# Optimization experiments

Hardware: AMD Instinct MI355X
Metric: run time of the kernel (lower is better)

The kernel has to match this reference:

```python
import jax, jax.numpy as jnp
import numpy as np

TIME_LEN = 8
JOINT_NUM = 22
SEQ = TIME_LEN * JOINT_NUM  # 176
H_NUM = 8
H_DIM = 32
NEG_BIG = -9e15


def _temporal_mask():
    # ones everywhere, except block-diagonal joint x joint blocks zeroed, plus identity
    m = np.ones((SEQ, SEQ), dtype=np.float32)
    for i in range(TIME_LEN):
        m[i * JOINT_NUM:(i + 1) * JOINT_NUM, i * JOINT_NUM:(i + 1) * JOINT_NUM] = 0.0
    spatial = 1.0 - m
    temporal = m + np.eye(SEQ, dtype=np.float32)
    return jnp.asarray(temporal), jnp.asarray(spatial)


def setup_inputs() -> dict:
    key = jax.random.key(0)
    ks = jax.random.split(key, 4)
    B, S, D_in = 256, SEQ, 128
    D_model = H_NUM * H_DIM
    s = 1.0 / np.sqrt(D_in)
    return {
        "x": jax.random.normal(ks[0], (B, S, D_in), dtype=jnp.float32),
        "Wq": jax.random.normal(ks[1], (D_in, D_model), dtype=jnp.float32) * s,
        "bq": jnp.zeros((D_model,), dtype=jnp.float32),
        "Wk": jax.random.normal(ks[2], (D_in, D_model), dtype=jnp.float32) * s,
        "bk": jnp.zeros((D_model,), dtype=jnp.float32),
        "Wv": jax.random.normal(ks[3], (D_in, D_model), dtype=jnp.float32) * s,
        "bv": jnp.zeros((D_model,), dtype=jnp.float32),
    }


def reference(x, Wq, bq, Wk, bk, Wv, bv):
    B = x.shape[0]
    mask, _ = _temporal_mask()  # att_type == 'temporal'

    def split_heads(t):  # [B,S,H*D] -> [B,H,S,D]
        return t.reshape(B, SEQ, H_NUM, H_DIM).transpose(0, 2, 1, 3)

    q = split_heads(x @ Wq + bq)
    k = split_heads(x @ Wk + bk)
    v = split_heads(jax.nn.relu(x @ Wv + bv))  # value map has ReLU

    scores = jnp.einsum("bhsd,bhtd->bhst", q, k) / jnp.sqrt(jnp.float32(H_DIM))
    scores = scores * mask + (1.0 - mask) * NEG_BIG
    att = jax.nn.softmax(scores, axis=-1)
    out = jnp.einsum("bhst,bhtd->bhsd", att, v)
    return out.transpose(0, 2, 1, 3).reshape(B, SEQ, H_NUM * H_DIM)
```

## Files before the change

kernel.cpp:

```cpp
#include <hip/hip_runtime.h>


#define SEQ    176
#define HD     32
#define DIN    128
#define DMODEL 256

typedef unsigned short ushort_t;
typedef __attribute__((ext_vector_type(8))) short short8;
typedef __attribute__((ext_vector_type(4))) short short4v;
typedef __attribute__((ext_vector_type(4))) float float4v;
typedef __attribute__((ext_vector_type(4))) unsigned short ushort4v;

#define WS_WT 0u
#define WS_X  196608u

#define SMEM_TOTAL 26496
#define OFF_KS 13056
#define OFF_VT 20096

__device__ __forceinline__ ushort_t f2bf(float f) {
    union { float f; unsigned int u; } cv; cv.f = f;
    unsigned int u = cv.u;
    unsigned int rb = 0x7FFFu + ((u >> 16) & 1u);
    return (ushort_t)((u + rb) >> 16);
}

__global__ __launch_bounds__(256)
void k0_conv(const float* __restrict__ x,
             const float* __restrict__ Wq, const float* __restrict__ Wk,
             const float* __restrict__ Wv,
             ushort_t* __restrict__ WT, ushort_t* __restrict__ X16)
{
    int bid = blockIdx.x;
    if (bid < 5632) {
        int f4 = bid * 256 + threadIdx.x;
        float4 v = reinterpret_cast<const float4*>(x)[f4];
        ushort4v o;
        o.x = f2bf(v.x); o.y = f2bf(v.y); o.z = f2bf(v.z); o.w = f2bf(v.w);
        reinterpret_cast<ushort4v*>(X16)[f4] = o;
    } else {
        int idx = (bid - 5632) * 256 + threadIdx.x;
        int e = idx * 4;
        int mat = e >> 15, h = (e >> 12) & 7, n = (e >> 7) & 31, k = e & 127;
        const float* W = (mat == 0) ? Wq : ((mat == 1) ? Wk : Wv);
        ushort4v o;
        o.x = f2bf(W[(k + 0) * DMODEL + h * HD + n]);
        o.y = f2bf(W[(k + 1) * DMODEL + h * HD + n]);
        o.z = f2bf(W[(k + 2) * DMODEL + h * HD + n]);
        o.w = f2bf(W[(k + 3) * DMODEL + h * HD + n]);
        reinterpret_cast<ushort4v*>(WT)[idx] = o;
    }
}

__global__ __launch_bounds__(704, 6)
void k1_attn(const ushort_t* __restrict__ X16, const ushort_t* __restrict__ WT,
             const float* __restrict__ bq, const float* __restrict__ bk,
             const float* __restrict__ bv, float* __restrict__ out)
{
    __shared__ ushort_t smem[SMEM_TOTAL];
    ushort_t* WS = smem;
    ushort_t* KS = smem + OFF_KS;
    ushort_t* VT = smem + OFF_VT;

    const int tid  = threadIdx.x;
    const int lane = tid & 63;
    const int w    = tid >> 6;
    const int c    = lane & 15;
    const int q    = lane >> 4;
    const int b    = blockIdx.x >> 3;
    const int h    = blockIdx.x & 7;

#pragma unroll
    for (int it = 0; it < 3; ++it) {
        int c8 = tid + it * 704;
        if (c8 < 1536) {
            int mat = c8 >> 9, rem = c8 & 511, n = rem >> 4, kc = rem & 15;
            short8 v = *reinterpret_cast<const short8*>(
                WT + (size_t)(((mat * 8 + h) * 32 + n) * 128 + kc * 8));
            *reinterpret_cast<short8*>(WS + (mat * 32 + n) * 136 + kc * 8) = v;
        }
    }
    if (tid < 512) {
        VT[(tid >> 4) * 200 + 176 + (tid & 15)] = 0;
    }
    __syncthreads();

    const ushort_t* xr = X16 + ((size_t)b * SEQ + w * 16 + c) * DIN;
    short8 xf[4];
#pragma unroll
    for (int kk = 0; kk < 4; ++kk)
        xf[kk] = *reinterpret_cast<const short8*>(xr + kk * 32 + q * 8);

    const float qscale = 0.17677669529663687f * 1.4426950408889634f;

    short8 qf8;
#pragma unroll
    for (int nt = 0; nt < 2; ++nt) {
        const ushort_t* wrow = WS + (nt * 16 + c) * 136 + q * 8;
        float4v acc = {0.f, 0.f, 0.f, 0.f};
#pragma unroll
        for (int kk = 0; kk < 4; ++kk) {
            short8 wf = *reinterpret_cast<const short8*>(wrow + kk * 32);
            acc = __builtin_amdgcn_mfma_f32_16x16x32_bf16(wf, xf[kk], acc, 0, 0, 0);
        }
        float4 bb = *reinterpret_cast<const float4*>(bq + h * HD + nt * 16 + q * 4);
        qf8[nt * 4 + 0] = (short)f2bf((acc[0] + bb.x) * qscale);
        qf8[nt * 4 + 1] = (short)f2bf((acc[1] + bb.y) * qscale);
        qf8[nt * 4 + 2] = (short)f2bf((acc[2] + bb.z) * qscale);
        qf8[nt * 4 + 3] = (short)f2bf((acc[3] + bb.w) * qscale);
    }
#pragma unroll
    for (int nt = 0; nt < 2; ++nt) {
        const ushort_t* wrow = WS + (32 + nt * 16 + c) * 136 + q * 8;
        float4v acc = {0.f, 0.f, 0.f, 0.f};
#pragma unroll
        for (int kk = 0; kk < 4; ++kk) {
            short8 wf = *reinterpret_cast<const short8*>(wrow + kk * 32);
            acc = __builtin_amdgcn_mfma_f32_16x16x32_bf16(xf[kk], wf, acc, 0, 0, 0);
        }
        float bia = bk[h * HD + nt * 16 + c];
#pragma unroll
        for (int r = 0; r < 4; ++r)
            KS[(w * 16 + q * 4 + r) * 40 + nt * 16 + c] = f2bf(acc[r] + bia);
    }
#pragma unroll
    for (int nt = 0; nt < 2; ++nt) {
        const ushort_t* wrow = WS + (64 + nt * 16 + c) * 136 + q * 8;
        float4v acc = {0.f, 0.f, 0.f, 0.f};
#pragma unroll
        for (int kk = 0; kk < 4; ++kk) {
            short8 wf = *reinterpret_cast<const short8*>(wrow + kk * 32);
            acc = __builtin_amdgcn_mfma_f32_16x16x32_bf16(wf, xf[kk], acc, 0, 0, 0);
        }
        float4 bb = *reinterpret_cast<const float4*>(bv + h * HD + nt * 16 + q * 4);
#pragma unroll
        for (int r = 0; r < 4; ++r) {
            float bias_r = (r == 0) ? bb.x : (r == 1) ? bb.y : (r == 2) ? bb.z : bb.w;
            float v = acc[r] + bias_r;
            v = v > 0.f ? v : 0.f;
            VT[(nt * 16 + q * 4 + r) * 200 + w * 16 + c] = f2bf(v);
        }
    }
    __syncthreads();

    const int t_row = w * 16 + c;
    const int lo = (t_row / 22) * 22;
    float su = 0.f;
    short8 pf[6];
    pf[5] = (short8){0, 0, 0, 0, 0, 0, 0, 0};
#pragma unroll
    for (int n = 0; n < 11; ++n) {
        const ushort_t* krow = KS + (n * 16 + c) * 40;
        short4v ka = *reinterpret_cast<const short4v*>(krow + q * 4);
        short4v kb = *reinterpret_cast<const short4v*>(krow + 16 + q * 4);
        short8 kf = {ka.x, ka.y, ka.z, ka.w, kb.x, kb.y, kb.z, kb.w};
        float4v s = {0.f, 0.f, 0.f, 0.f};
        s = __builtin_amdgcn_mfma_f32_16x16x32_bf16(kf, qf8, s, 0, 0, 0);
#pragma unroll
        for (int r = 0; r < 4; ++r) {
            int tp = n * 16 + q * 4 + r;
            float sv = (((unsigned)(tp - lo) < 22u) && (tp != t_row)) ? -1e30f : s[r];
            float e = __builtin_amdgcn_exp2f(sv);
            su += e;
            pf[n >> 1][(n & 1) * 4 + r] = (short)f2bf(e);
        }
    }
    su += __shfl_xor(su, 16, 64);
    su += __shfl_xor(su, 32, 64);
    const float invs = 1.0f / su;

    float* ob = out + ((size_t)b * SEQ + t_row) * DMODEL + h * HD;
#pragma unroll
    for (int mt = 0; mt < 2; ++mt) {
        const ushort_t* vrow = VT + (mt * 16 + c) * 200;
        float4v o = {0.f, 0.f, 0.f, 0.f};
#pragma unroll
        for (int g = 0; g < 6; ++g) {
            short4v va = *reinterpret_cast<const short4v*>(vrow + (2 * g) * 16 + q * 4);
            short4v vb = *reinterpret_cast<const short4v*>(vrow + (2 * g + 1) * 16 + q * 4);
            short8 vf = {va.x, va.y, va.z, va.w, vb.x, vb.y, vb.z, vb.w};
            o = __builtin_amdgcn_mfma_f32_16x16x32_bf16(vf, pf[g], o, 0, 0, 0);
        }
        float4 st;
        st.x = o[0] * invs; st.y = o[1] * invs;
        st.z = o[2] * invs; st.w = o[3] * invs;
        *reinterpret_cast<float4*>(ob + mt * 16 + q * 4) = st;
    }
}

extern "C" void kernel_launch(void* const* d_in, const int* in_sizes, int n_in,
                              void* d_out, int out_size, void* d_ws, size_t ws_size,
                              hipStream_t stream) {
    const float* x  = (const float*)d_in[0];
    const float* Wq = (const float*)d_in[1];
    const float* bq = (const float*)d_in[2];
    const float* Wk = (const float*)d_in[3];
    const float* bk = (const float*)d_in[4];
    const float* Wv = (const float*)d_in[5];
    const float* bv = (const float*)d_in[6];
    float* out = (float*)d_out;

    char* ws = (char*)d_ws;
    ushort_t* WT  = (ushort_t*)(ws + WS_WT);
    ushort_t* X16 = (ushort_t*)(ws + WS_X);

    k0_conv<<<dim3(5728), dim3(256), 0, stream>>>(x, Wq, Wk, Wv, WT, X16);
    k1_attn<<<dim3(2048), dim3(704), 0, stream>>>(X16, WT, bq, bk, bv, out);
}
```

Measured before the change: 133.4 us.

## Process two batches per block and swizzle K/V smem layout for 128-bit reads

Each block now handles two batch elements for one head, so the per-head weight tile is staged into shared memory once and the weight fragments are reused across both batches. K and V^T are stored with a permuted column layout so the score and PV stages can fetch each MFMA operand with a single 16-byte LDS load instead of two 8-byte loads. The grid is halved and shared memory per block grows from about 53KB to about 80KB. That may cut resident blocks per CU and adds register pressure from doubled x fragments.

```diff
diff --git a/kernel.cpp b/kernel.cpp
--- a/kernel.cpp
+++ b/kernel.cpp
@@ -15,9 +15,11 @@
 #define WS_WT 0u
 #define WS_X  196608u
 
-#define SMEM_TOTAL 26496
+#define SMEM_TOTAL 39936
 #define OFF_KS 13056
-#define OFF_VT 20096
+#define OFF_VT 27136
+#define KS_B   7040
+#define VT_B   6400
 
 __device__ __forceinline__ ushort_t f2bf(float f) {
     union { float f; unsigned int u; } cv; cv.f = f;
@@ -68,7 +70,7 @@
     const int w    = tid >> 6;
     const int c    = lane & 15;
     const int q    = lane >> 4;
-    const int b    = blockIdx.x >> 3;
+    const int b0   = (blockIdx.x >> 3) * 2;
     const int h    = blockIdx.x & 7;
 
 #pragma unroll
@@ -82,110 +84,118 @@
         }
     }
     if (tid < 512) {
-        VT[(tid >> 4) * 200 + 176 + (tid & 15)] = 0;
+        int bb = tid >> 8, rem = tid & 255;
+        int row = rem >> 3, ch = rem & 7;
+        short4v z = {0, 0, 0, 0};
+        *reinterpret_cast<short4v*>(VT + bb * VT_B + row * 200 + 160 + ch * 4) = z;
     }
     __syncthreads();
 
-    const ushort_t* xr = X16 + ((size_t)b * SEQ + w * 16 + c) * DIN;
-    short8 xf[4];
-#pragma unroll
-    for (int kk = 0; kk < 4; ++kk)
-        xf[kk] = *reinterpret_cast<const short8*>(xr + kk * 32 + q * 8);
+    short8 xf[2][4];
+#pragma unroll
+    for (int bb = 0; bb < 2; ++bb) {
+        const ushort_t* xr = X16 + ((size_t)(b0 + bb) * SEQ + w * 16 + c) * DIN;
+#pragma unroll
+        for (int kk = 0; kk < 4; ++kk)
+            xf[bb][kk] = *reinterpret_cast<const short8*>(xr + kk * 32 + q * 8);
+    }
 
     const float qscale = 0.17677669529663687f * 1.4426950408889634f;
-
-    short8 qf8;
-#pragma unroll
-    for (int nt = 0; nt < 2; ++nt) {
-        const ushort_t* wrow = WS + (nt * 16 + c) * 136 + q * 8;
-        float4v acc = {0.f, 0.f, 0.f, 0.f};
-#pragma unroll
-        for (int kk = 0; kk < 4; ++kk) {
-            short8 wf = *reinterpret_cast<const short8*>(wrow + kk * 32);
-            acc = __builtin_amdgcn_mfma_f32_16x16x32_bf16(wf, xf[kk], acc, 0, 0, 0);
-        }
-        float4 bb = *reinterpret_cast<const float4*>(bq + h * HD + nt * 16 + q * 4);
-        qf8[nt * 4 + 0] = (short)f2bf((acc[0] + bb.x) * qscale);
-        qf8[nt * 4 + 1] = (short)f2bf((acc[1] + bb.y) * qscale);
-        qf8[nt * 4 + 2] = (short)f2bf((acc[2] + bb.z) * qscale);
-        qf8[nt * 4 + 3] = (short)f2bf((acc[3] + bb.w) * qscale);
-    }
-#pragma unroll
-    for (int nt = 0; nt < 2; ++nt) {
-        const ushort_t* wrow = WS + (32 + nt * 16 + c) * 136 + q * 8;
-        float4v acc = {0.f, 0.f, 0.f, 0.f};
-#pragma unroll
-        for (int kk = 0; kk < 4; ++kk) {
-            short8 wf = *reinterpret_cast<const short8*>(wrow + kk * 32);
-            acc = __builtin_amdgcn_mfma_f32_16x16x32_bf16(xf[kk], wf, acc, 0, 0, 0);
-        }
-        float bia = bk[h * HD + nt * 16 + c];
-#pragma unroll
-        for (int r = 0; r < 4; ++r)
-            KS[(w * 16 + q * 4 + r) * 40 + nt * 16 + c] = f2bf(acc[r] + bia);
-    }
-#pragma unroll
-    for (int nt = 0; nt < 2; ++nt) {
-        const ushort_t* wrow = WS + (64 + nt * 16 + c) * 136 + q * 8;
-        float4v acc = {0.f, 0.f, 0.f, 0.f};
-#pragma unroll
-        for (int kk = 0; kk < 4; ++kk) {
-            short8 wf = *reinterpret_cast<const short8*>(wrow + kk * 32);
-            acc = __builtin_amdgcn_mfma_f32_16x16x32_bf16(wf, xf[kk], acc, 0, 0, 0);
-        }
-        float4 bb = *reinterpret_cast<const float4*>(bv + h * HD + nt * 16 + q * 4);
-#pragma unroll
-        for (int r = 0; r < 4; ++r) {
-            float bias_r = (r == 0) ? bb.x : (r == 1) ? bb.y : (r == 2) ? bb.z : bb.w;
-            float v = acc[r] + bias_r;
-            v = v > 0.f ? v : 0.f;
-            VT[(nt * 16 + q * 4 + r) * 200 + w * 16 + c] = f2bf(v);
+    short8 qf8[2];
+    const int skv = (c >> 2) * 8 + (c & 3);
+    const int svt = (w >> 1) * 32 + (c >> 2) * 8 + (w & 1) * 4 + (c & 3);
+
+#pragma unroll
+    for (int jj = 0; jj < 6; ++jj) {
+        const int mat = jj >> 1, nt = jj & 1;
+        const ushort_t* wrow = WS + (mat * 32 + nt * 16 + c) * 136 + q * 8;
+        short8 wf[4];
+#pragma unroll
+        for (int kk = 0; kk < 4; ++kk)
+            wf[kk] = *reinterpret_cast<const short8*>(wrow + kk * 32);
+
+#pragma unroll
+        for (int bb = 0; bb < 2; ++bb) {
+            float4v acc = {0.f, 0.f, 0.f, 0.f};
+            if (mat == 1) {
+#pragma unroll
+                for (int kk = 0; kk < 4; ++kk)
+                    acc = __builtin_amdgcn_mfma_f32_16x16x32_bf16(xf[bb][kk], wf[kk], acc, 0, 0, 0);
+            } else {
+#pragma unroll
+                for (int kk = 0; kk < 4; ++kk)
+                    acc = __builtin_amdgcn_mfma_f32_16x16x32_bf16(wf[kk], xf[bb][kk], acc, 0, 0, 0);
+            }
+            if (mat == 0) {
+                float4 bb4 = *reinterpret_cast<const float4*>(bq + h * HD + nt * 16 + q * 4);
+                qf8[bb][nt * 4 + 0] = (short)f2bf((acc[0] + bb4.x) * qscale);
+                qf8[bb][nt * 4 + 1] = (short)f2bf((acc[1] + bb4.y) * qscale);
+                qf8[bb][nt * 4 + 2] = (short)f2bf((acc[2] + bb4.z) * qscale);
+                qf8[bb][nt * 4 + 3] = (short)f2bf((acc[3] + bb4.w) * qscale);
+            } else if (mat == 1) {
+                float bia = bk[h * HD + nt * 16 + c];
+                ushort_t* ksb = KS + bb * KS_B;
+#pragma unroll
+                for (int r = 0; r < 4; ++r)
+                    ksb[(w * 16 + q * 4 + r) * 40 + skv + nt * 4] = f2bf(acc[r] + bia);
+            } else {
+                float4 bb4 = *reinterpret_cast<const float4*>(bv + h * HD + nt * 16 + q * 4);
+                ushort_t* vtb = VT + bb * VT_B;
+#pragma unroll
+                for (int r = 0; r < 4; ++r) {
+                    float bias_r = (r == 0) ? bb4.x : (r == 1) ? bb4.y : (r == 2) ? bb4.z : bb4.w;
+                    float v = acc[r] + bias_r;
+                    v = v > 0.f ? v : 0.f;
+                    vtb[(nt * 16 + q * 4 + r) * 200 + svt] = f2bf(v);
+                }
+            }
         }
     }
     __syncthreads();
 
     const int t_row = w * 16 + c;
     const int lo = (t_row / 22) * 22;
-    float su = 0.f;
-    short8 pf[6];
-    pf[5] = (short8){0, 0, 0, 0, 0, 0, 0, 0};
-#pragma unroll
-    for (int n = 0; n < 11; ++n) {
-        const ushort_t* krow = KS + (n * 16 + c) * 40;
-        short4v ka = *reinterpret_cast<const short4v*>(krow + q * 4);
-        short4v kb = *reinterpret_cast<const short4v*>(krow + 16 + q * 4);
-        short8 kf = {ka.x, ka.y, ka.z, ka.w, kb.x, kb.y, kb.z, kb.w};
-        float4v s = {0.f, 0.f, 0.f, 0.f};
-        s = __builtin_amdgcn_mfma_f32_16x16x32_bf16(kf, qf8, s, 0, 0, 0);
-#pragma unroll
-        for (int r = 0; r < 4; ++r) {
-            int tp = n * 16 + q * 4 + r;
-            float sv = (((unsigned)(tp - lo) < 22u) && (tp != t_row)) ? -1e30f : s[r];
-            float e = __builtin_amdgcn_exp2f(sv);
-            su += e;
-            pf[n >> 1][(n & 1) * 4 + r] = (short)f2bf(e);
-        }
-    }
-    su += __shfl_xor(su, 16, 64);
-    su += __shfl_xor(su, 32, 64);
-    const float invs = 1.0f / su;
-
-    float* ob = out + ((size_t)b * SEQ + t_row) * DMODEL + h * HD;
-#pragma unroll
-    for (int mt = 0; mt < 2; ++mt) {
-        const ushort_t* vrow = VT + (mt * 16 + c) * 200;
-        float4v o = {0.f, 0.f, 0.f, 0.f};
-#pragma unroll
-        for (int g = 0; g < 6; ++g) {
-            short4v va = *reinterpret_cast<const short4v*>(vrow + (2 * g) * 16 + q * 4);
-            short4v vb = *reinterpret_cast<const short4v*>(vrow + (2 * g + 1) * 16 + q * 4);
-            short8 vf = {va.x, va.y, va.z, va.w, vb.x, vb.y, vb.z, vb.w};
-            o = __builtin_amdgcn_mfma_f32_16x16x32_bf16(vf, pf[g], o, 0, 0, 0);
-        }
-        float4 st;
-        st.x = o[0] * invs; st.y = o[1] * invs;
-        st.z = o[2] * invs; st.w = o[3] * invs;
-        *reinterpret_cast<float4*>(ob + mt * 16 + q * 4) = st;
+
+#pragma unroll
+    for (int bb = 0; bb < 2; ++bb) {
+        const ushort_t* KSb = KS + bb * KS_B;
+        const ushort_t* VTb = VT + bb * VT_B;
+        float su = 0.f;
+        short8 pf[6];
+        pf[5] = (short8){0, 0, 0, 0, 0, 0, 0, 0};
+#pragma unroll
+        for (int n = 0; n < 11; ++n) {
+            short8 kf = *reinterpret_cast<const short8*>(KSb + (n * 16 + c) * 40 + q * 8);
+            float4v s = {0.f, 0.f, 0.f, 0.f};
+            s = __builtin_amdgcn_mfma_f32_16x16x32_bf16(kf, qf8[bb], s, 0, 0, 0);
+#pragma unroll
+            for (int r = 0; r < 4; ++r) {
+                int tp = n * 16 + q * 4 + r;
+                float sv = (((unsigned)(tp - lo) < 22u) && (tp != t_row)) ? -1e30f : s[r];
+                float e = __builtin_amdgcn_exp2f(sv);
+                su += e;
+                pf[n >> 1][(n & 1) * 4 + r] = (short)f2bf(e);
+            }
+        }
+        su += __shfl_xor(su, 16, 64);
+        su += __shfl_xor(su, 32, 64);
+        const float invs = 1.0f / su;
+
+        float* ob = out + ((size_t)(b0 + bb) * SEQ + t_row) * DMODEL + h * HD;
+#pragma unroll
+        for (int mt = 0; mt < 2; ++mt) {
+            const ushort_t* vrow = VTb + (mt * 16 + c) * 200;
+            float4v o = {0.f, 0.f, 0.f, 0.f};
+#pragma unroll
+            for (int g = 0; g < 6; ++g) {
+                short8 vf = *reinterpret_cast<const short8*>(vrow + g * 32 + q * 8);
+                o = __builtin_amdgcn_mfma_f32_16x16x32_bf16(vf, pf[g], o, 0, 0, 0);
+            }
+            float4 st;
+            st.x = o[0] * invs; st.y = o[1] * invs;
+            st.z = o[2] * invs; st.w = o[3] * invs;
+            *reinterpret_cast<float4*>(ob + mt * 16 + q * 4) = st;
+        }
     }
 }
 
@@ -206,5 +216,5 @@
     ushort_t* X16 = (ushort_t*)(ws + WS_X);
 
     k0_conv<<<dim3(5728), dim3(256), 0, stream>>>(x, Wq, Wk, Wv, WT, X16);
-    k1_attn<<<dim3(2048), dim3(704), 0, stream>>>(X16, WT, bq, bk, bv, out);
-}
+    k1_attn<<<dim3(1024), dim3(704), 0, stream>>>(X16, WT, bq, bk, bv, out);
+}
```

New measurement: 135.9 us. No clear change (+1.8%).

## Shrink attention blocks to 8 waves, read weights from global, permute K/V LDS layout

Applied to the files above, without the earlier changes.

The attention kernel now runs 512-thread blocks. Each wave handles up to two 16-row tiles, with the 11 tiles spread over 8 waves. The per-block LDS copy of the weight slices is dropped, and weights are read directly from global/L2, roughly halving shared memory per block. K and V are stored in a permuted LDS layout so that score and PV fragments load as single 16-byte reads instead of two 8-byte reads. Blocks are reordered so consecutive blocks share a head, and a cheaper round-half-up bf16 conversion is used inside the attention kernel. The trade-off is less balanced work (some waves do two tiles, others one) and more global weight traffic in exchange for higher occupancy and fewer LDS operations.

```diff
diff --git a/kernel.cpp b/kernel.cpp
--- a/kernel.cpp
+++ b/kernel.cpp
@@ -15,15 +15,18 @@
 #define WS_WT 0u
 #define WS_X  196608u
 
-#define SMEM_TOTAL 26496
-#define OFF_KS 13056
-#define OFF_VT 20096
-
-__device__ __forceinline__ ushort_t f2bf(float f) {
+#define SMEM_TOTAL 13440
+#define OFF_VT 7040
+
+__device__ __forceinline__ ushort_t f2bf_rtne(float f) {
     union { float f; unsigned int u; } cv; cv.f = f;
     unsigned int u = cv.u;
     unsigned int rb = 0x7FFFu + ((u >> 16) & 1u);
     return (ushort_t)((u + rb) >> 16);
+}
+__device__ __forceinline__ ushort_t f2bf(float f) {
+    union { float f; unsigned int u; } cv; cv.f = f;
+    return (ushort_t)((cv.u + 0x8000u) >> 16);
 }
 
 __global__ __launch_bounds__(256)
@@ -37,7 +40,8 @@
         int f4 = bid * 256 + threadIdx.x;
         float4 v = reinterpret_cast<const float4*>(x)[f4];
         ushort4v o;
-        o.x = f2bf(v.x); o.y = f2bf(v.y); o.z = f2bf(v.z); o.w = f2bf(v.w);
+        o.x = f2bf_rtne(v.x); o.y = f2bf_rtne(v.y);
+        o.z = f2bf_rtne(v.z); o.w = f2bf_rtne(v.w);
         reinterpret_cast<ushort4v*>(X16)[f4] = o;
     } else {
         int idx = (bid - 5632) * 256 + threadIdx.x;
@@ -45,147 +49,140 @@
         int mat = e >> 15, h = (e >> 12) & 7, n = (e >> 7) & 31, k = e & 127;
         const float* W = (mat == 0) ? Wq : ((mat == 1) ? Wk : Wv);
         ushort4v o;
-        o.x = f2bf(W[(k + 0) * DMODEL + h * HD + n]);
-        o.y = f2bf(W[(k + 1) * DMODEL + h * HD + n]);
-        o.z = f2bf(W[(k + 2) * DMODEL + h * HD + n]);
-        o.w = f2bf(W[(k + 3) * DMODEL + h * HD + n]);
+        o.x = f2bf_rtne(W[(k + 0) * DMODEL + h * HD + n]);
+        o.y = f2bf_rtne(W[(k + 1) * DMODEL + h * HD + n]);
+        o.z = f2bf_rtne(W[(k + 2) * DMODEL + h * HD + n]);
+        o.w = f2bf_rtne(W[(k + 3) * DMODEL + h * HD + n]);
         reinterpret_cast<ushort4v*>(WT)[idx] = o;
     }
 }
 
-__global__ __launch_bounds__(704, 6)
+__global__ __launch_bounds__(512, 8)
 void k1_attn(const ushort_t* __restrict__ X16, const ushort_t* __restrict__ WT,
              const float* __restrict__ bq, const float* __restrict__ bk,
              const float* __restrict__ bv, float* __restrict__ out)
 {
     __shared__ ushort_t smem[SMEM_TOTAL];
-    ushort_t* WS = smem;
-    ushort_t* KS = smem + OFF_KS;
+    ushort_t* KS = smem;
     ushort_t* VT = smem + OFF_VT;
 
     const int tid  = threadIdx.x;
     const int lane = tid & 63;
-    const int w    = tid >> 6;
+    const int wave = tid >> 6;
     const int c    = lane & 15;
     const int q    = lane >> 4;
-    const int b    = blockIdx.x >> 3;
-    const int h    = blockIdx.x & 7;
-
-#pragma unroll
-    for (int it = 0; it < 3; ++it) {
-        int c8 = tid + it * 704;
-        if (c8 < 1536) {
-            int mat = c8 >> 9, rem = c8 & 511, n = rem >> 4, kc = rem & 15;
-            short8 v = *reinterpret_cast<const short8*>(
-                WT + (size_t)(((mat * 8 + h) * 32 + n) * 128 + kc * 8));
-            *reinterpret_cast<short8*>(WS + (mat * 32 + n) * 136 + kc * 8) = v;
+    const int b    = blockIdx.x & 255;
+    const int h    = blockIdx.x >> 8;
+
+    {
+        int row = tid >> 4, m = tid & 15;
+        VT[row * 200 + 160 + (m >> 2) * 8 + 4 + (m & 3)] = 0;
+    }
+
+    const float qscale = 0.17677669529663687f * 1.4426950408889634f;
+    const int skv = (c >> 2) * 8 + (c & 3);
+    short8 qf8[2];
+
+#pragma unroll
+    for (int it = 0; it < 2; ++it) {
+        const int mt = wave + it * 8;
+        if (mt < 11) {
+            const ushort_t* xr = X16 + ((size_t)b * SEQ + mt * 16 + c) * DIN;
+            short8 xf[4];
+#pragma unroll
+            for (int kk = 0; kk < 4; ++kk)
+                xf[kk] = *reinterpret_cast<const short8*>(xr + kk * 32 + q * 8);
+            const int svt = (mt >> 1) * 32 + (c >> 2) * 8 + (mt & 1) * 4 + (c & 3);
+
+#pragma unroll
+            for (int jj = 0; jj < 6; ++jj) {
+                const int mat = jj >> 1, nt = jj & 1;
+                const ushort_t* wrow =
+                    WT + (size_t)(((mat * 8 + h) * 32 + nt * 16 + c)) * 128 + q * 8;
+                float4v acc = {0.f, 0.f, 0.f, 0.f};
+                if (mat == 1) {
+#pragma unroll
+                    for (int kk = 0; kk < 4; ++kk) {
+                        short8 wf = *reinterpret_cast<const short8*>(wrow + kk * 32);
+                        acc = __builtin_amdgcn_mfma_f32_16x16x32_bf16(xf[kk], wf, acc, 0, 0, 0);
+                    }
+                } else {
+#pragma unroll
+                    for (int kk = 0; kk < 4; ++kk) {
+                        short8 wf = *reinterpret_cast<const short8*>(wrow + kk * 32);
+                        acc = __builtin_amdgcn_mfma_f32_16x16x32_bf16(wf, xf[kk], acc, 0, 0, 0);
+                    }
+                }
+                if (mat == 0) {
+                    float4 bb4 = *reinterpret_cast<const float4*>(bq + h * HD + nt * 16 + q * 4);
+                    qf8[it][nt * 4 + 0] = (short)f2bf((acc[0] + bb4.x) * qscale);
+                    qf8[it][nt * 4 + 1] = (short)f2bf((acc[1] + bb4.y) * qscale);
+                    qf8[it][nt * 4 + 2] = (short)f2bf((acc[2] + bb4.z) * qscale);
+                    qf8[it][nt * 4 + 3] = (short)f2bf((acc[3] + bb4.w) * qscale);
+                } else if (mat == 1) {
+                    float bia = bk[h * HD + nt * 16 + c];
+#pragma unroll
+                    for (int r = 0; r < 4; ++r)
+                        KS[(mt * 16 + q * 4 + r) * 40 + skv + nt * 4] = f2bf(acc[r] + bia);
+                } else {
+                    float4 bb4 = *reinterpret_cast<const float4*>(bv + h * HD + nt * 16 + q * 4);
+#pragma unroll
+                    for (int r = 0; r < 4; ++r) {
+                        float bias_r = (r == 0) ? bb4.x : (r == 1) ? bb4.y
+                                      : (r == 2) ? bb4.z : bb4.w;
+                        float v = acc[r] + bias_r;
+                        v = v > 0.f ? v : 0.f;
+                        VT[(nt * 16 + q * 4 + r) * 200 + svt] = f2bf(v);
+                    }
+                }
+            }
         }
     }
-    if (tid < 512) {
-        VT[(tid >> 4) * 200 + 176 + (tid & 15)] = 0;
-    }
     __syncthreads();
 
-    const ushort_t* xr = X16 + ((size_t)b * SEQ + w * 16 + c) * DIN;
-    short8 xf[4];
-#pragma unroll
-    for (int kk = 0; kk < 4; ++kk)
-        xf[kk] = *reinterpret_cast<const short8*>(xr + kk * 32 + q * 8);
-
-    const float qscale = 0.17677669529663687f * 1.4426950408889634f;
-
-    short8 qf8;
-#pragma unroll
-    for (int nt = 0; nt < 2; ++nt) {
-        const ushort_t* wrow = WS + (nt * 16 + c) * 136 + q * 8;
-        float4v acc = {0.f, 0.f, 0.f, 0.f};
-#pragma unroll
-        for (int kk = 0; kk < 4; ++kk) {
-            short8 wf = *reinterpret_cast<const short8*>(wrow + kk * 32);
-            acc = __builtin_amdgcn_mfma_f32_16x16x32_bf16(wf, xf[kk], acc, 0, 0, 0);
+#pragma unroll
+    for (int it = 0; it < 2; ++it) {
+        const int rt = wave + it * 8;
+        if (rt < 11) {
+            const int t_row = rt * 16 + c;
+            const int lo = (t_row / 22) * 22;
+            float su = 0.f;
+            short8 pf[6];
+            pf[5] = (short8){0, 0, 0, 0, 0, 0, 0, 0};
+#pragma unroll
+            for (int n = 0; n < 11; ++n) {
+                short8 kf = *reinterpret_cast<const short8*>(KS + (n * 16 + c) * 40 + q * 8);
+                float4v s = {0.f, 0.f, 0.f, 0.f};
+                s = __builtin_amdgcn_mfma_f32_16x16x32_bf16(kf, qf8[it], s, 0, 0, 0);
+#pragma unroll
+                for (int r = 0; r < 4; ++r) {
+                    int tp = n * 16 + q * 4 + r;
+                    float sv = (((unsigned)(tp - lo) < 22u) && (tp != t_row)) ? -1e30f : s[r];
+                    float e = __builtin_amdgcn_exp2f(sv);
+                    su += e;
+                    pf[n >> 1][(n & 1) * 4 + r] = (short)f2bf(e);
+                }
+            }
+            su += __shfl_xor(su, 16, 64);
+            su += __shfl_xor(su, 32, 64);
+            const float invs = 1.0f / su;
+
+            float* ob = out + ((size_t)b * SEQ + t_row) * DMODEL + h * HD;
+#pragma unroll
+            for (int mt2 = 0; mt2 < 2; ++mt2) {
+                const ushort_t* vrow = VT + (mt2 * 16 + c) * 200;
+                float4v o = {0.f, 0.f, 0.f, 0.f};
+#pragma unroll
+                for (int g = 0; g < 6; ++g) {
+                    short8 vf = *reinterpret_cast<const short8*>(vrow + g * 32 + q * 8);
+                    o = __builtin_amdgcn_mfma_f32_16x16x32_bf16(vf, pf[g], o, 0, 0, 0);
+                }
+                float4 st;
+                st.x = o[0] * invs; st.y = o[1] * invs;
+                st.z = o[2] * invs; st.w = o[3] * invs;
+                *reinterpret_cast<float4*>(ob + mt2 * 16 + q * 4) = st;
+            }
         }
-        float4 bb = *reinterpret_cast<const float4*>(bq + h * HD + nt * 16 + q * 4);
-        qf8[nt * 4 + 0] = (short)f2bf((acc[0] + bb.x) * qscale);
-        qf8[nt * 4 + 1] = (short)f2bf((acc[1] + bb.y) * qscale);
-        qf8[nt * 4 + 2] = (short)f2bf((acc[2] + bb.z) * qscale);
-        qf8[nt * 4 + 3] = (short)f2bf((acc[3] + bb.w) * qscale);
-    }
-#pragma unroll
-    for (int nt = 0; nt < 2; ++nt) {
-        const ushort_t* wrow = WS + (32 + nt * 16 + c) * 136 + q * 8;
-        float4v acc = {0.f, 0.f, 0.f, 0.f};
-#pragma unroll
-        for (int kk = 0; kk < 4; ++kk) {
-            short8 wf = *reinterpret_cast<const short8*>(wrow + kk * 32);
-            acc = __builtin_amdgcn_mfma_f32_16x16x32_bf16(xf[kk], wf, acc, 0, 0, 0);
-        }
-        float bia = bk[h * HD + nt * 16 + c];
-#pragma unroll
-        for (int r = 0; r < 4; ++r)
-            KS[(w * 16 + q * 4 + r) * 40 + nt * 16 + c] = f2bf(acc[r] + bia);
-    }
-#pragma unroll
-    for (int nt = 0; nt < 2; ++nt) {
-        const ushort_t* wrow = WS + (64 + nt * 16 + c) * 136 + q * 8;
-        float4v acc = {0.f, 0.f, 0.f, 0.f};
-#pragma unroll
-        for (int kk = 0; kk < 4; ++kk) {
-            short8 wf = *reinterpret_cast<const short8*>(wrow + kk * 32);
-            acc = __builtin_amdgcn_mfma_f32_16x16x32_bf16(wf, xf[kk], acc, 0, 0, 0);
-        }
-        float4 bb = *reinterpret_cast<const float4*>(bv + h * HD + nt * 16 + q * 4);
-#pragma unroll
-        for (int r = 0; r < 4; ++r) {
-            float bias_r = (r == 0) ? bb.x : (r == 1) ? bb.y : (r == 2) ? bb.z : bb.w;
-            float v = acc[r] + bias_r;
-            v = v > 0.f ? v : 0.f;
-            VT[(nt * 16 + q * 4 + r) * 200 + w * 16 + c] = f2bf(v);
-        }
-    }
-    __syncthreads();
-
-    const int t_row = w * 16 + c;
-    const int lo = (t_row / 22) * 22;
-    float su = 0.f;
-    short8 pf[6];
-    pf[5] = (short8){0, 0, 0, 0, 0, 0, 0, 0};
-#pragma unroll
-    for (int n = 0; n < 11; ++n) {
-        const ushort_t* krow = KS + (n * 16 + c) * 40;
-        short4v ka = *reinterpret_cast<const short4v*>(krow + q * 4);
-        short4v kb = *reinterpret_cast<const short4v*>(krow + 16 + q * 4);
-        short8 kf = {ka.x, ka.y, ka.z, ka.w, kb.x, kb.y, kb.z, kb.w};
-        float4v s = {0.f, 0.f, 0.f, 0.f};
-        s = __builtin_amdgcn_mfma_f32_16x16x32_bf16(kf, qf8, s, 0, 0, 0);
-#pragma unroll
-        for (int r = 0; r < 4; ++r) {
-            int tp = n * 16 + q * 4 + r;
-            float sv = (((unsigned)(tp - lo) < 22u) && (tp != t_row)) ? -1e30f : s[r];
-            float e = __builtin_amdgcn_exp2f(sv);
-            su += e;
-            pf[n >> 1][(n & 1) * 4 + r] = (short)f2bf(e);
-        }
-    }
-    su += __shfl_xor(su, 16, 64);
-    su += __shfl_xor(su, 32, 64);
-    const float invs = 1.0f / su;
-
-    float* ob = out + ((size_t)b * SEQ + t_row) * DMODEL + h * HD;
-#pragma unroll
-    for (int mt = 0; mt < 2; ++mt) {
-        const ushort_t* vrow = VT + (mt * 16 + c) * 200;
-        float4v o = {0.f, 0.f, 0.f, 0.f};
-#pragma unroll
-        for (int g = 0; g < 6; ++g) {
-            short4v va = *reinterpret_cast<const short4v*>(vrow + (2 * g) * 16 + q * 4);
-            short4v vb = *reinterpret_cast<const short4v*>(vrow + (2 * g + 1) * 16 + q * 4);
-            short8 vf = {va.x, va.y, va.z, va.w, vb.x, vb.y, vb.z, vb.w};
-            o = __builtin_amdgcn_mfma_f32_16x16x32_bf16(vf, pf[g], o, 0, 0, 0);
-        }
-        float4 st;
-        st.x = o[0] * invs; st.y = o[1] * invs;
-        st.z = o[2] * invs; st.w = o[3] * invs;
-        *reinterpret_cast<float4*>(ob + mt * 16 + q * 4) = st;
     }
 }
 
@@ -206,5 +203,5 @@
     ushort_t* X16 = (ushort_t*)(ws + WS_X);
 
     k0_conv<<<dim3(5728), dim3(256), 0, stream>>>(x, Wq, Wk, Wv, WT, X16);
-    k1_attn<<<dim3(2048), dim3(704), 0, stream>>>(X16, WT, bq, bk, bv, out);
-}
+    k1_attn<<<dim3(2048), dim3(512), 0, stream>>>(X16, WT, bq, bk, bv, out);
+}
```

Result: slower. 199.0 us (+49.2%).
